# Kernel tuning notes

Hardware: AMD Instinct MI355X
Metric: run time of the kernel (lower is better)

## Reference

```python
import jax, jax.numpy as jnp
import numpy as np

K = 512          # num_embeddings
D = 8            # latent_dim
DECAY = 0.99     # ema_decay
EPS = 1e-5


def setup_inputs() -> dict:
    key = jax.random.key(0)
    k1, k2 = jax.random.split(key)
    z = jax.random.normal(k1, (64, D, 64, 64), dtype=jnp.float32)
    # codebook initialized uniform(-1/K, 1/K) as in the torch module
    codebook = jax.random.uniform(k2, (K, D), dtype=jnp.float32,
                                  minval=-1.0 / K, maxval=1.0 / K)
    ema_cluster_size = jnp.zeros((K,), dtype=jnp.float32)
    ema_w = jnp.zeros((K, D), dtype=jnp.float32)
    return {"z": z, "codebook": codebook,
            "ema_cluster_size": ema_cluster_size, "ema_w": ema_w}


def reference(z, codebook, ema_cluster_size, ema_w):
    B, C, H, W = z.shape
    # (B, HW, C) flattened latents, matching z.view(B,C,-1).permute(0,2,1)
    flat = z.reshape(B, C, H * W).transpose(0, 2, 1)

    # cdist p=2: ||z||^2 - 2 z.e + ||e||^2, then sqrt (argmin unaffected,
    # but we keep the sqrt for faithfulness to torch.cdist)
    z_sq = jnp.sum(flat * flat, axis=-1, keepdims=True)        # (B, N, 1)
    e_sq = jnp.sum(codebook * codebook, axis=-1)               # (K,)
    dots = jnp.einsum('bnd,kd->bnk', flat, codebook)           # (B, N, K)
    distances = jnp.sqrt(jnp.maximum(z_sq - 2.0 * dots + e_sq, 0.0))

    indices = jnp.argmin(distances, axis=-1)                   # (B, N) int

    # embedding gather with the OLD codebook (as in the torch forward)
    z_q = codebook[indices]                                    # (B, N, D)
    z_q = z_q.transpose(0, 2, 1).reshape(B, C, H, W)

    commitment_loss = jnp.mean((jax.lax.stop_gradient(z_q) - z) ** 2)
    loss = commitment_loss  # use_ema=True branch

    # ---- EMA in-place codebook update (buffers) ----
    idx_flat = indices.reshape(-1)                             # (B*N,)
    inp_flat = flat.reshape(-1, C)                             # (B*N, D)
    counts = jax.ops.segment_sum(jnp.ones_like(idx_flat, dtype=z.dtype),
                                 idx_flat, num_segments=K)     # (K,)
    sums = jax.ops.segment_sum(inp_flat, idx_flat, num_segments=K)  # (K, D)

    new_cs = ema_cluster_size * DECAY + counts * (1.0 - DECAY)
    new_w = ema_w * DECAY + sums * (1.0 - DECAY)
    n = jnp.sum(new_cs)
    cs_smoothed = (new_cs + EPS) / (n + K * EPS) * n
    new_codebook = new_w / cs_smoothed[:, None]

    return z_q, loss, new_codebook, cs_smoothed, new_w
```

## Files before the change

kernel.cpp:

```cpp
#include <hip/hip_runtime.h>

constexpr int Kc   = 512;
constexpr int Dc   = 8;
constexpr int HWc  = 4096;
constexpr int CHWc = Dc * HWc;
constexpr int Mc   = 64 * HWc;
constexpr int TOTALc = Mc * Dc;

constexpr int REP      = 8;
constexpr int RSTRIDE  = 4616;
constexpr int ACC_FLOATS = REP * RSTRIDE;

__global__ __launch_bounds__(256) void vq_prep(const float* __restrict__ cb,
                                               float* __restrict__ ws) {
    const int tid = blockIdx.x * 256 + threadIdx.x;
    float4* w4 = (float4*)ws;
    for (int i = tid; i < ACC_FLOATS / 4; i += gridDim.x * 256)
        w4[i] = float4{0.f, 0.f, 0.f, 0.f};
    if (blockIdx.x == 0) {
        for (int k = threadIdx.x; k < Kc; k += 256) {
            float s = 0.f;
#pragma unroll
            for (int c = 0; c < Dc; ++c) {
                const float e = cb[k * Dc + c];
                s = fmaf(e, e, s);
            }
            ws[ACC_FLOATS + k] = s;
        }
    }
}

__global__ __launch_bounds__(512, 8) void vq_main(const float* __restrict__ z,
                                                  const float* __restrict__ cb,
                                                  const float* __restrict__ esq,
                                                  float* __restrict__ ws,
                                                  float* __restrict__ zq) {
    __shared__ float s_counts[Kc];
    __shared__ float s_sums[Kc * Dc];
    __shared__ float s_mn[4][256];
    __shared__ int   s_im[4][256];
    __shared__ float s_loss;

    const int t = threadIdx.x;
    for (int i = t; i < Kc; i += 512) s_counts[i] = 0.f;
    for (int i = t; i < Kc * Dc; i += 512) s_sums[i] = 0.f;
    if (t == 0) s_loss = 0.f;

    const int vl = t & 127;
    const int g  = __builtin_amdgcn_readfirstlane(t >> 7);
    const int k0 = g << 7;

    const int base = blockIdx.x * 256;
    const int n0 = (base + vl) & (HWc - 1);
    const int b  = base >> 12;
    const float* zb = z + b * CHWc + n0;

    float zz0[Dc], zz1[Dc];
#pragma unroll
    for (int c = 0; c < Dc; ++c) {
        zz0[c] = -2.0f * zb[c * HWc];
        zz1[c] = -2.0f * zb[c * HWc + 128];
    }

    float mn0 = 3.4e38f, mn1 = 3.4e38f;
    int   i0 = k0, i1 = k0;
#pragma unroll 4
    for (int kk = 0; kk < 128; ++kk) {
        const int k = k0 + kk;
        float a0 = esq[k];
        float a1 = a0;
#pragma unroll
        for (int c = 0; c < Dc; ++c) {
            const float e = cb[k * Dc + c];
            a0 = fmaf(zz0[c], e, a0);
            a1 = fmaf(zz1[c], e, a1);
        }
        const bool c0 = a0 < mn0;
        mn0 = c0 ? a0 : mn0;
        i0  = c0 ? k  : i0;
        const bool c1 = a1 < mn1;
        mn1 = c1 ? a1 : mn1;
        i1  = c1 ? k  : i1;
    }
    s_mn[g][vl]       = mn0;
    s_im[g][vl]       = i0;
    s_mn[g][vl + 128] = mn1;
    s_im[g][vl + 128] = i1;
    __syncthreads();

    if (t < 256) {
        const int v = t;
        float mn = s_mn[0][v];
        int   im = s_im[0][v];
#pragma unroll
        for (int gg = 1; gg < 4; ++gg) {
            const float m2 = s_mn[gg][v];
            const int   j2 = s_im[gg][v];
            const bool  c2 = m2 < mn;
            mn = c2 ? m2 : mn;
            im = c2 ? j2 : im;
        }

        const float4* cb4 = (const float4*)cb;
        const float4 qa = cb4[im * 2], qb = cb4[im * 2 + 1];
        const float q[Dc] = {qa.x, qa.y, qa.z, qa.w, qb.x, qb.y, qb.z, qb.w};

        const int nv = (base + v) & (HWc - 1);
        const float* zv = z + b * CHWc + nv;
        float* zqv = zq + b * CHWc + nv;
        float lsum = 0.f;
        float zr[Dc];
#pragma unroll
        for (int c = 0; c < Dc; ++c) {
            zr[c] = zv[c * HWc];
            zqv[c * HWc] = q[c];
            const float d = q[c] - zr[c];
            lsum = fmaf(d, d, lsum);
        }

        unsafeAtomicAdd(&s_counts[im], 1.0f);
#pragma unroll
        for (int c = 0; c < Dc; ++c)
            unsafeAtomicAdd(&s_sums[im * Dc + c], zr[c]);
        unsafeAtomicAdd(&s_loss, lsum);
    }
    __syncthreads();

    float* acc = ws + (blockIdx.x & (REP - 1)) * RSTRIDE;
    for (int i = t; i < Kc; i += 512) {
        const float val = s_counts[i];
        if (val != 0.f) unsafeAtomicAdd(&acc[i], val);
    }
    for (int i = t; i < Kc * Dc; i += 512) {
        const float val = s_sums[i];
        if (val != 0.f) unsafeAtomicAdd(&acc[512 + i], val);
    }
    if (t == 0) unsafeAtomicAdd(&acc[4608], s_loss);
}

__global__ __launch_bounds__(512) void vq_final(const float* __restrict__ ws,
                                                const float* __restrict__ ema_cs,
                                                const float* __restrict__ ema_w,
                                                float* __restrict__ out) {
    constexpr float DEC  = 0.99f;
    constexpr float OMD  = (float)(1.0 - 0.99);
    constexpr float EPSf = 1e-5f;
    constexpr float KEPS = (float)(512 * 1e-5);
    __shared__ float red[512];
    __shared__ float s_cs[512];

    const int t = threadIdx.x;
    float cnt = 0.f;
#pragma unroll
    for (int r = 0; r < REP; ++r) cnt += ws[r * RSTRIDE + t];
    const float ncs = ema_cs[t] * DEC + cnt * OMD;
    red[t] = ncs;
    __syncthreads();
    for (int s = 256; s > 0; s >>= 1) {
        if (t < s) red[t] += red[t + s];
        __syncthreads();
    }
    const float n  = red[0];
    const float cs = (ncs + EPSf) / (n + KEPS) * n;
    s_cs[t] = cs;

    float* out_loss = out + TOTALc;
    float* out_cb   = out + TOTALc + 1;
    float* out_cs   = out_cb + Kc * Dc;
    float* out_nw   = out_cs + Kc;

    out_cs[t] = cs;
    __syncthreads();

    for (int e = t; e < Kc * Dc; e += 512) {
        float sm = 0.f;
#pragma unroll
        for (int r = 0; r < REP; ++r) sm += ws[r * RSTRIDE + 512 + e];
        const float nw = ema_w[e] * DEC + sm * OMD;
        out_nw[e] = nw;
        out_cb[e] = nw / s_cs[e >> 3];
    }
    if (t == 0) {
        float ls = 0.f;
#pragma unroll
        for (int r = 0; r < REP; ++r) ls += ws[r * RSTRIDE + 4608];
        out_loss[0] = ls * (1.0f / 2097152.0f);
    }
}

extern "C" void kernel_launch(void* const* d_in, const int* in_sizes, int n_in,
                              void* d_out, int out_size, void* d_ws, size_t ws_size,
                              hipStream_t stream) {
    const float* z      = (const float*)d_in[0];
    const float* cb     = (const float*)d_in[1];
    const float* ema_cs = (const float*)d_in[2];
    const float* ema_w  = (const float*)d_in[3];
    float* out = (float*)d_out;
    float* ws  = (float*)d_ws;

    vq_prep<<<32, 256, 0, stream>>>(cb, ws);
    vq_main<<<Mc / 256, 512, 0, stream>>>(z, cb, ws + ACC_FLOATS, ws, out);
    vq_final<<<1, 512, 0, stream>>>(ws, ema_cs, ema_w, out);
}
```

Before: 112.4 us.

## Use packed float2 FMAs and 8 codebook groups with 4 vectors per thread

The distance search is re-split so each wave handles 64 codebook entries against 4 latent vectors per lane instead of 128 entries against 2. The dot products use packed 2-wide float vector math (v_pk_fma) with the squared norm stored as a padded float2, which halves the FMA instruction count. This doubles per-thread register use for the latent vectors and the cross-group min reduction grows from 4 to 8 stages. The split dimension pairs add one extra horizontal add per comparison.

Measured after the change: 115.8 us. 3.1% more time.

```diff
diff --git a/kernel.cpp b/kernel.cpp
--- a/kernel.cpp
+++ b/kernel.cpp
@@ -6,6 +6,8 @@
 constexpr int CHWc = Dc * HWc;
 constexpr int Mc   = 64 * HWc;
 constexpr int TOTALc = Mc * Dc;
+
+typedef float v2f __attribute__((ext_vector_type(2)));
 
 constexpr int REP      = 8;
 constexpr int RSTRIDE  = 4616;
@@ -25,20 +27,21 @@
                 const float e = cb[k * Dc + c];
                 s = fmaf(e, e, s);
             }
-            ws[ACC_FLOATS + k] = s;
+            ws[ACC_FLOATS + 2 * k]     = s;
+            ws[ACC_FLOATS + 2 * k + 1] = 0.f;
         }
     }
 }
 
 __global__ __launch_bounds__(512, 8) void vq_main(const float* __restrict__ z,
                                                   const float* __restrict__ cb,
-                                                  const float* __restrict__ esq,
+                                                  const float* __restrict__ esqw,
                                                   float* __restrict__ ws,
                                                   float* __restrict__ zq) {
     __shared__ float s_counts[Kc];
     __shared__ float s_sums[Kc * Dc];
-    __shared__ float s_mn[4][256];
-    __shared__ int   s_im[4][256];
+    __shared__ float s_mn[8][256];
+    __shared__ int   s_im[8][256];
     __shared__ float s_loss;
 
     const int t = threadIdx.x;
@@ -46,63 +49,71 @@
     for (int i = t; i < Kc * Dc; i += 512) s_sums[i] = 0.f;
     if (t == 0) s_loss = 0.f;
 
-    const int vl = t & 127;
-    const int g  = __builtin_amdgcn_readfirstlane(t >> 7);
-    const int k0 = g << 7;
+    const int l = t & 63;
+    const int g  = __builtin_amdgcn_readfirstlane(t >> 6);
+    const int k0 = g << 6;
 
     const int base = blockIdx.x * 256;
-    const int n0 = (base + vl) & (HWc - 1);
+    const int n0 = (base + l) & (HWc - 1);
     const int b  = base >> 12;
     const float* zb = z + b * CHWc + n0;
 
-    float zz0[Dc], zz1[Dc];
-#pragma unroll
-    for (int c = 0; c < Dc; ++c) {
-        zz0[c] = -2.0f * zb[c * HWc];
-        zz1[c] = -2.0f * zb[c * HWc + 128];
-    }
-
-    float mn0 = 3.4e38f, mn1 = 3.4e38f;
-    int   i0 = k0, i1 = k0;
+    v2f zzp[4][4];
+#pragma unroll
+    for (int j = 0; j < 4; ++j)
+#pragma unroll
+        for (int p = 0; p < 4; ++p) {
+            zzp[j][p].x = -2.0f * zb[(2 * p)     * HWc + 64 * j];
+            zzp[j][p].y = -2.0f * zb[(2 * p + 1) * HWc + 64 * j];
+        }
+
+    const v2f* cb2  = (const v2f*)cb;
+    const v2f* esq2 = (const v2f*)esqw;
+
+    float mn[4] = {3.4e38f, 3.4e38f, 3.4e38f, 3.4e38f};
+    int   im[4] = {k0, k0, k0, k0};
 #pragma unroll 4
-    for (int kk = 0; kk < 128; ++kk) {
+    for (int kk = 0; kk < 64; ++kk) {
         const int k = k0 + kk;
-        float a0 = esq[k];
-        float a1 = a0;
-#pragma unroll
-        for (int c = 0; c < Dc; ++c) {
-            const float e = cb[k * Dc + c];
-            a0 = fmaf(zz0[c], e, a0);
-            a1 = fmaf(zz1[c], e, a1);
-        }
-        const bool c0 = a0 < mn0;
-        mn0 = c0 ? a0 : mn0;
-        i0  = c0 ? k  : i0;
-        const bool c1 = a1 < mn1;
-        mn1 = c1 ? a1 : mn1;
-        i1  = c1 ? k  : i1;
-    }
-    s_mn[g][vl]       = mn0;
-    s_im[g][vl]       = i0;
-    s_mn[g][vl + 128] = mn1;
-    s_im[g][vl + 128] = i1;
+        const v2f e0 = cb2[k * 4 + 0];
+        const v2f e1 = cb2[k * 4 + 1];
+        const v2f e2 = cb2[k * 4 + 2];
+        const v2f e3 = cb2[k * 4 + 3];
+        const v2f eq = esq2[k];
+#pragma unroll
+        for (int j = 0; j < 4; ++j) {
+            v2f acc = zzp[j][0] * e0 + eq;
+            acc = zzp[j][1] * e1 + acc;
+            acc = zzp[j][2] * e2 + acc;
+            acc = zzp[j][3] * e3 + acc;
+            const float a = acc.x + acc.y;
+            const bool cm = a < mn[j];
+            mn[j] = cm ? a : mn[j];
+            im[j] = cm ? k : im[j];
+        }
+    }
+#pragma unroll
+    for (int j = 0; j < 4; ++j) {
+        s_mn[g][l + 64 * j] = mn[j];
+        s_im[g][l + 64 * j] = im[j];
+    }
     __syncthreads();
 
     if (t < 256) {
         const int v = t;
-        float mn = s_mn[0][v];
-        int   im = s_im[0][v];
-#pragma unroll
-        for (int gg = 1; gg < 4; ++gg) {
+        float mnv = s_mn[0][v];
+        int   imv = s_im[0][v];
+#pragma unroll
+        for (int gg = 1; gg < 8; ++gg) {
             const float m2 = s_mn[gg][v];
             const int   j2 = s_im[gg][v];
-            const bool  c2 = m2 < mn;
-            mn = c2 ? m2 : mn;
-            im = c2 ? j2 : im;
+            const bool  c2 = m2 < mnv;
+            mnv = c2 ? m2 : mnv;
+            imv = c2 ? j2 : imv;
         }
 
         const float4* cb4 = (const float4*)cb;
-        const float4 qa = cb4[im * 2], qb = cb4[im * 2 + 1];
+        const float4 qa = cb4[imv * 2], qb = cb4[imv * 2 + 1];
         const float q[Dc] = {qa.x, qa.y, qa.z, qa.w, qb.x, qb.y, qb.z, qb.w};
 
         const int nv = (base + v) & (HWc - 1);
@@ -118,10 +129,10 @@
             lsum = fmaf(d, d, lsum);
         }
 
-        unsafeAtomicAdd(&s_counts[im], 1.0f);
+        unsafeAtomicAdd(&s_counts[imv], 1.0f);
 #pragma unroll
         for (int c = 0; c < Dc; ++c)
-            unsafeAtomicAdd(&s_sums[im * Dc + c], zr[c]);
+            unsafeAtomicAdd(&s_sums[imv * Dc + c], zr[c]);
         unsafeAtomicAdd(&s_loss, lsum);
     }
     __syncthreads();
```

## Fuse final EMA reduction into main kernel via last-block completion counter

Applied to the files above, without the earlier changes.

Removes the separate vq_final launch by having every vq_main block increment a global atomic counter after flushing its partial sums. The last block to arrive then performs the EMA codebook update itself. Also reuses the z values already held in registers instead of reloading z for the loss and sums, and zeroes shared memory with float4 stores. This saves a kernel launch and its gap, at the cost of a threadfence and an atomic in every block.

New measurement: 246.3 us. +119.1%, slower.

```diff
diff --git a/kernel.cpp b/kernel.cpp
--- a/kernel.cpp
+++ b/kernel.cpp
@@ -27,24 +27,34 @@
             }
             ws[ACC_FLOATS + k] = s;
         }
+        if (threadIdx.x == 0)
+            ((unsigned*)ws)[ACC_FLOATS + 512] = 0u;
     }
 }
 
 __global__ __launch_bounds__(512, 8) void vq_main(const float* __restrict__ z,
                                                   const float* __restrict__ cb,
                                                   const float* __restrict__ esq,
+                                                  const float* __restrict__ ema_cs,
+                                                  const float* __restrict__ ema_w,
                                                   float* __restrict__ ws,
-                                                  float* __restrict__ zq) {
-    __shared__ float s_counts[Kc];
-    __shared__ float s_sums[Kc * Dc];
+                                                  float* __restrict__ out) {
+    __shared__ __align__(16) float s_counts[Kc];
+    __shared__ __align__(16) float s_sums[Kc * Dc];
     __shared__ float s_mn[4][256];
     __shared__ int   s_im[4][256];
     __shared__ float s_loss;
+    __shared__ int   s_last;
 
     const int t = threadIdx.x;
-    for (int i = t; i < Kc; i += 512) s_counts[i] = 0.f;
-    for (int i = t; i < Kc * Dc; i += 512) s_sums[i] = 0.f;
-    if (t == 0) s_loss = 0.f;
+    {
+        const float4 z4 = {0.f, 0.f, 0.f, 0.f};
+        float4* sc4 = (float4*)s_counts;
+        float4* ss4 = (float4*)s_sums;
+        if (t < 128) sc4[t] = z4;
+        for (int i = t; i < Kc * Dc / 4; i += 512) ss4[i] = z4;
+        if (t == 0) s_loss = 0.f;
+    }
 
     const int vl = t & 127;
     const int g  = __builtin_amdgcn_readfirstlane(t >> 7);
@@ -90,100 +100,116 @@
 
     if (t < 256) {
         const int v = t;
-        float mn = s_mn[0][v];
-        int   im = s_im[0][v];
+        float mnv = s_mn[0][v];
+        int   imv = s_im[0][v];
 #pragma unroll
         for (int gg = 1; gg < 4; ++gg) {
             const float m2 = s_mn[gg][v];
             const int   j2 = s_im[gg][v];
-            const bool  c2 = m2 < mn;
-            mn = c2 ? m2 : mn;
-            im = c2 ? j2 : im;
-        }
+            const bool  c2 = m2 < mnv;
+            mnv = c2 ? m2 : mnv;
+            imv = c2 ? j2 : imv;
+        }
+
+        float zr[Dc];
+#pragma unroll
+        for (int c = 0; c < Dc; ++c)
+            zr[c] = -0.5f * ((t < 128) ? zz0[c] : zz1[c]);
 
         const float4* cb4 = (const float4*)cb;
-        const float4 qa = cb4[im * 2], qb = cb4[im * 2 + 1];
+        const float4 qa = cb4[imv * 2], qb = cb4[imv * 2 + 1];
         const float q[Dc] = {qa.x, qa.y, qa.z, qa.w, qb.x, qb.y, qb.z, qb.w};
 
         const int nv = (base + v) & (HWc - 1);
-        const float* zv = z + b * CHWc + nv;
-        float* zqv = zq + b * CHWc + nv;
+        float* zqv = out + b * CHWc + nv;
         float lsum = 0.f;
-        float zr[Dc];
 #pragma unroll
         for (int c = 0; c < Dc; ++c) {
-            zr[c] = zv[c * HWc];
             zqv[c * HWc] = q[c];
             const float d = q[c] - zr[c];
             lsum = fmaf(d, d, lsum);
         }
 
-        unsafeAtomicAdd(&s_counts[im], 1.0f);
+        unsafeAtomicAdd(&s_counts[imv], 1.0f);
 #pragma unroll
         for (int c = 0; c < Dc; ++c)
-            unsafeAtomicAdd(&s_sums[im * Dc + c], zr[c]);
+            unsafeAtomicAdd(&s_sums[imv * Dc + c], zr[c]);
         unsafeAtomicAdd(&s_loss, lsum);
     }
     __syncthreads();
 
-    float* acc = ws + (blockIdx.x & (REP - 1)) * RSTRIDE;
-    for (int i = t; i < Kc; i += 512) {
-        const float val = s_counts[i];
-        if (val != 0.f) unsafeAtomicAdd(&acc[i], val);
-    }
-    for (int i = t; i < Kc * Dc; i += 512) {
-        const float val = s_sums[i];
-        if (val != 0.f) unsafeAtomicAdd(&acc[512 + i], val);
-    }
-    if (t == 0) unsafeAtomicAdd(&acc[4608], s_loss);
-}
-
-__global__ __launch_bounds__(512) void vq_final(const float* __restrict__ ws,
-                                                const float* __restrict__ ema_cs,
-                                                const float* __restrict__ ema_w,
-                                                float* __restrict__ out) {
+    {
+        float* acc = ws + (blockIdx.x & (REP - 1)) * RSTRIDE;
+        for (int i = t; i < Kc; i += 512) {
+            const float val = s_counts[i];
+            if (val != 0.f) unsafeAtomicAdd(&acc[i], val);
+        }
+        for (int i = t; i < Kc * Dc; i += 512) {
+            const float val = s_sums[i];
+            if (val != 0.f) unsafeAtomicAdd(&acc[512 + i], val);
+        }
+        if (t == 0) unsafeAtomicAdd(&acc[4608], s_loss);
+    }
+
+    __threadfence();
+    __syncthreads();
+    if (t == 0) {
+        unsigned* ctr = (unsigned*)(ws + ACC_FLOATS + 512);
+        const unsigned old = __hip_atomic_fetch_add(ctr, 1u, __ATOMIC_ACQ_REL,
+                                                    __HIP_MEMORY_SCOPE_AGENT);
+        s_last = (old == gridDim.x - 1) ? 1 : 0;
+    }
+    __syncthreads();
+    if (s_last == 0) return;
+    __threadfence();
+
     constexpr float DEC  = 0.99f;
     constexpr float OMD  = (float)(1.0 - 0.99);
     constexpr float EPSf = 1e-5f;
     constexpr float KEPS = (float)(512 * 1e-5);
-    __shared__ float red[512];
-    __shared__ float s_cs[512];
-
-    const int t = threadIdx.x;
+    float* s_ncs = &s_mn[0][0];
+
     float cnt = 0.f;
 #pragma unroll
-    for (int r = 0; r < REP; ++r) cnt += ws[r * RSTRIDE + t];
+    for (int r = 0; r < REP; ++r)
+        cnt += __hip_atomic_load(&ws[r * RSTRIDE + t], __ATOMIC_RELAXED,
+                                 __HIP_MEMORY_SCOPE_AGENT);
     const float ncs = ema_cs[t] * DEC + cnt * OMD;
-    red[t] = ncs;
+    s_ncs[t]    = ncs;
+    s_counts[t] = ncs;
     __syncthreads();
     for (int s = 256; s > 0; s >>= 1) {
-        if (t < s) red[t] += red[t + s];
+        if (t < s) s_counts[t] += s_counts[t + s];
         __syncthreads();
     }
-    const float n  = red[0];
-    const float cs = (ncs + EPSf) / (n + KEPS) * n;
-    s_cs[t] = cs;
+    const float n = s_counts[0];
 
     float* out_loss = out + TOTALc;
     float* out_cb   = out + TOTALc + 1;
     float* out_cs   = out_cb + Kc * Dc;
     float* out_nw   = out_cs + Kc;
 
-    out_cs[t] = cs;
-    __syncthreads();
+    out_cs[t] = (ncs + EPSf) / (n + KEPS) * n;
 
     for (int e = t; e < Kc * Dc; e += 512) {
+        const float ncs_k = s_ncs[e >> 3];
+        const float cs_k  = (ncs_k + EPSf) / (n + KEPS) * n;
         float sm = 0.f;
 #pragma unroll
-        for (int r = 0; r < REP; ++r) sm += ws[r * RSTRIDE + 512 + e];
+        for (int r = 0; r < REP; ++r)
+            sm += __hip_atomic_load(&ws[r * RSTRIDE + 512 + e],
+                                    __ATOMIC_RELAXED,
+                                    __HIP_MEMORY_SCOPE_AGENT);
         const float nw = ema_w[e] * DEC + sm * OMD;
         out_nw[e] = nw;
-        out_cb[e] = nw / s_cs[e >> 3];
+        out_cb[e] = nw / cs_k;
     }
     if (t == 0) {
         float ls = 0.f;
 #pragma unroll
-        for (int r = 0; r < REP; ++r) ls += ws[r * RSTRIDE + 4608];
+        for (int r = 0; r < REP; ++r)
+            ls += __hip_atomic_load(&ws[r * RSTRIDE + 4608], __ATOMIC_RELAXED,
+                                    __HIP_MEMORY_SCOPE_AGENT);
         out_loss[0] = ls * (1.0f / 2097152.0f);
     }
 }
@@ -199,6 +225,6 @@
     float* ws  = (float*)d_ws;
 
     vq_prep<<<32, 256, 0, stream>>>(cb, ws);
-    vq_main<<<Mc / 256, 512, 0, stream>>>(z, cb, ws + ACC_FLOATS, ws, out);
-    vq_final<<<1, 512, 0, stream>>>(ws, ema_cs, ema_w, out);
+    vq_main<<<Mc / 256, 512, 0, stream>>>(z, cb, ws + ACC_FLOATS,
+                                          ema_cs, ema_w, ws, out);
 }
```
